# Performance work log

Hardware: AMD Instinct MI355X
Metric: run time of the kernel (lower is better)

Reference implementation:

```python
import jax, jax.numpy as jnp
import numpy as np

N_LAYERS = 3
FEATS = 128
POS = 3
M_DIM = 64
E_IN = 1 + 2 * FEATS          # 257 (rel_dist + x_i + x_j)
N_NODES = 20000
N_EDGES = 320000
LN_EPS = 1e-5


def _xavier(key, shape):
    fan_in, fan_out = shape[0], shape[1]
    std = (2.0 / (fan_in + fan_out)) ** 0.5
    return jax.random.normal(key, shape, dtype=jnp.float32) * std


def setup_inputs() -> dict:
    key = jax.random.key(0)
    ks = jax.random.split(key, 10)
    x = jax.random.normal(ks[0], (N_NODES, POS + FEATS), dtype=jnp.float32)
    edge_index = jax.random.randint(ks[1], (2, N_EDGES), 0, N_NODES)
    L = N_LAYERS
    def stack(k, shape):
        return jax.vmap(lambda kk: _xavier(kk, shape))(jax.random.split(k, L))
    params = {
        "ew1": stack(ks[2], (E_IN, 2 * E_IN)),      # edge_mlp linear 1
        "eb1": jnp.zeros((L, 2 * E_IN), jnp.float32),
        "ew2": stack(ks[3], (2 * E_IN, M_DIM)),      # edge_mlp linear 2
        "eb2": jnp.zeros((L, M_DIM), jnp.float32),
        "ng": jnp.ones((L, FEATS), jnp.float32),     # node LayerNorm gamma
        "nb": jnp.zeros((L, FEATS), jnp.float32),    # node LayerNorm beta
        "nw1": stack(ks[4], (FEATS + M_DIM, 2 * FEATS)),
        "nb1": jnp.zeros((L, 2 * FEATS), jnp.float32),
        "nw2": stack(ks[5], (2 * FEATS, FEATS)),
        "nb2": jnp.zeros((L, FEATS), jnp.float32),
        "cw1": stack(ks[6], (M_DIM, 4 * M_DIM)),
        "cb1": jnp.zeros((L, 4 * M_DIM), jnp.float32),
        "cw2": stack(ks[7], (4 * M_DIM, 1)),
        "cb2": jnp.zeros((L, 1), jnp.float32),
    }
    return {"x": x, "edge_index": edge_index, **params}


def _layer(x, edge_index, ew1, eb1, ew2, eb2, ng, nb, nw1, nb1, nw2, nb2,
           cw1, cb1, cw2, cb2):
    coors, feats = x[:, :POS], x[:, POS:]
    src, dst = edge_index[0], edge_index[1]
    # relative geometry per edge
    rel_coors = coors[src] - coors[dst]                       # [E, 3]
    rel_dist = jnp.sum(rel_coors * rel_coors, axis=-1, keepdims=True)  # [E, 1]
    # message MLP: cat[x_i (target), x_j (source), rel_dist]
    e_in = jnp.concatenate([feats[dst], feats[src], rel_dist], axis=-1)
    h = jax.nn.silu(e_in @ ew1 + eb1)
    m_ij = jax.nn.silu(h @ ew2 + eb2)                         # [E, m_dim]
    # coordinate update
    coor_w = jax.nn.silu(m_ij @ cw1 + cb1) @ cw2 + cb2        # [E, 1]
    mhat = jax.ops.segment_sum(coor_w * rel_coors, dst, num_segments=N_NODES)
    coors_out = coors + mhat
    # feature update (LayerNorm then MLP, residual)
    m_i = jax.ops.segment_sum(m_ij, dst, num_segments=N_NODES)
    mu = jnp.mean(feats, axis=-1, keepdims=True)
    var = jnp.mean((feats - mu) ** 2, axis=-1, keepdims=True)
    feats_n = (feats - mu) * jax.lax.rsqrt(var + LN_EPS) * ng + nb
    n_in = jnp.concatenate([feats_n, m_i], axis=-1)
    nh = jax.nn.silu(n_in @ nw1 + nb1) @ nw2 + nb2
    feats_out = feats + nh
    return jnp.concatenate([coors_out, feats_out], axis=-1)


def reference(x, edge_index, ew1, eb1, ew2, eb2, ng, nb, nw1, nb1, nw2, nb2,
              cw1, cb1, cw2, cb2):
    for l in range(N_LAYERS):
        x = _layer(x, edge_index,
                   ew1[l], eb1[l], ew2[l], eb2[l],
                   ng[l], nb[l], nw1[l], nb1[l], nw2[l], nb2[l],
                   cw1[l], cb1[l], cw2[l], cb2[l])
    return x
```

## Files before the change

kernel.cpp:

```cpp
#include <hip/hip_runtime.h>

typedef unsigned short u16;
typedef unsigned int   u32;
typedef __attribute__((ext_vector_type(2))) u32  u32x2;
typedef __attribute__((ext_vector_type(4))) u32  u32x4;
typedef __attribute__((ext_vector_type(8))) __bf16 bf16x8;
typedef __attribute__((ext_vector_type(4))) float  f32x4;

#define NN 20000
#define NE 320000
#define XD 131
#define F  128
#define MD 64
#define H1 514
#define H1P 544
#define NCH 17

#define GAS __attribute__((address_space(1)))
#define LAS __attribute__((address_space(3)))
#define LGKM0 asm volatile("s_waitcnt lgkmcnt(0)" ::: "memory")
#define VM0   asm volatile("s_waitcnt vmcnt(0)" ::: "memory")

__device__ __forceinline__ float silu(float a) {
    float e = __expf(-a);
    return a * __builtin_amdgcn_rcpf(1.0f + e);
}

__device__ __forceinline__ u16 f2bf(float f) {
    u32 u = __builtin_bit_cast(u32, f);
    return (u16)((u + 0x7FFFu + ((u >> 16) & 1u)) >> 16);
}
__device__ __forceinline__ u16 bfc(float f) { return __builtin_bit_cast(u16, (__bf16)f); }
__device__ __forceinline__ u32 pk2(float a, float b) {
    return (u32)bfc(a) | ((u32)bfc(b) << 16);
}
__device__ __forceinline__ bf16x8 mk8(u32 a, u32 b, u32 c, u32 d) {
    u32x4 t = {a, b, c, d};
    return __builtin_bit_cast(bf16x8, t);
}
__device__ __forceinline__ f32x4 mfma16(bf16x8 a, bf16x8 b, f32x4 c) {
    return __builtin_amdgcn_mfma_f32_16x16x32_bf16(a, b, c, 0, 0, 0);
}


__global__ void prep_w1(const float* __restrict__ ew1, const float* __restrict__ eb1,
                        u16* __restrict__ w1b, float* __restrict__ bias2) {
    int i = blockIdx.x * 256 + threadIdx.x;
    if (i >= 3 * H1P * 256) return;
    int k = i & 255;
    int n = (i >> 8) % H1P;
    int l = (i >> 8) / H1P;
    float v = (n < H1) ? ew1[(size_t)l * 257 * H1 + (size_t)k * H1 + n] : 0.f;
    w1b[(size_t)(l * H1P + n) * 256 + (k ^ ((n & 7) << 3))] = f2bf(v);
    if (k == 0) {
        bias2[(l * H1P + n) * 2 + 0] = (n < H1) ? eb1[l * H1 + n] : 0.f;
        bias2[(l * H1P + n) * 2 + 1] = (n < H1) ? ew1[(size_t)l * 257 * H1 + (size_t)256 * H1 + n] : 0.f;
    }
}

__global__ void prep_w2(const float* __restrict__ ew2, u16* __restrict__ w2b) {
    int i = blockIdx.x * 256 + threadIdx.x;
    if (i >= 3 * 64 * H1P) return;
    int k = i % H1P;
    int n = (i / H1P) & 63;
    int l = i / (H1P * 64);
    float v = (k < H1) ? ew2[(size_t)l * H1 * 64 + (size_t)k * 64 + n] : 0.f;
    w2b[(size_t)(l * 64 + n) * H1P + k] = f2bf(v);
}

__global__ void prep_cw1(const float* __restrict__ cw1, u16* __restrict__ cw1b) {
    int i = blockIdx.x * 256 + threadIdx.x;
    if (i >= 3 * 256 * 64) return;
    int k = i & 63;
    int n = (i >> 6) & 255;
    int l = i >> 14;
    cw1b[(size_t)l * 16384 + n * 64 + k] = f2bf(cw1[(size_t)l * 16384 + k * 256 + n]);
}

__global__ void prep_nw1(const float* __restrict__ nw1, u16* __restrict__ nw1b) {
    int i = blockIdx.x * 256 + threadIdx.x;
    if (i >= 3 * 256 * 192) return;
    int k = i % 192;
    int n = (i / 192) & 255;
    int l = i / (192 * 256);
    nw1b[(size_t)(l * 256 + n) * 192 + k] = f2bf(nw1[(size_t)l * 192 * 256 + (size_t)k * 256 + n]);
}

__global__ void prep_nw2(const float* __restrict__ nw2, u16* __restrict__ nw2b) {
    int i = blockIdx.x * 256 + threadIdx.x;
    if (i >= 3 * 128 * 256) return;
    int k = i & 255;
    int n = (i >> 8) & 127;
    int l = i >> 15;
    nw2b[(size_t)(l * 128 + n) * 256 + k] = f2bf(nw2[(size_t)l * 256 * 128 + (size_t)k * 128 + n]);
}

__global__ void x2bf(const float* __restrict__ xc, u32* __restrict__ xbf) {
    int i = blockIdx.x * 256 + threadIdx.x;
    if (i >= NN * 64) return;
    const int node = i >> 6, p = i & 63;
    const float a = xc[(size_t)node * XD + 3 + 2 * p];
    const float b = xc[(size_t)node * XD + 4 + 2 * p];
    xbf[(size_t)node * 64 + p] = pk2(a, b);
}


__global__ void csr_hist(const int* __restrict__ eidx, int* __restrict__ cnt) {
    int e = blockIdx.x * 256 + threadIdx.x;
    if (e < NE) atomicAdd(&cnt[eidx[NE + e]], 1);
}

__global__ void csr_scan(const int* __restrict__ cnt, int* __restrict__ rowp) {
    __shared__ int ps[1024];
    const int t = threadIdx.x;
    const int base = t * 20;
    int loc[20];
    int s = 0;
    #pragma unroll
    for (int i = 0; i < 20; ++i) {
        const int idx = base + i;
        const int c = (idx < NN) ? cnt[idx] : 0;
        loc[i] = s;
        s += c;
    }
    ps[t] = s;
    __syncthreads();
    for (int off = 1; off < 1024; off <<= 1) {
        int v = (t >= off) ? ps[t - off] : 0;
        __syncthreads();
        ps[t] += v;
        __syncthreads();
    }
    const int segbase = (t > 0) ? ps[t - 1] : 0;
    #pragma unroll
    for (int i = 0; i < 20; ++i) {
        const int idx = base + i;
        if (idx < NN) rowp[idx] = segbase + loc[i];
    }
    if (t == 1023) rowp[NN] = ps[1023];
}

__global__ void csr_fill(const int* __restrict__ eidx, const int* __restrict__ rowp,
                         int* __restrict__ fill, int* __restrict__ eids) {
    int e = blockIdx.x * 256 + threadIdx.x;
    if (e >= NE) return;
    const int d = eidx[NE + e];
    const int pos = atomicAdd(&fill[d], 1);
    eids[rowp[d] + pos] = e;
}

__global__ void esort(const int* __restrict__ eidx, const int* __restrict__ eids,
                      int* __restrict__ esrc, int* __restrict__ edst) {
    int j = blockIdx.x * 256 + threadIdx.x;
    if (j >= NE) return;
    const int e = eids[j];
    esrc[j] = eidx[e];
    edst[j] = eidx[NE + e];
}


__global__ __launch_bounds__(256, 4) void reduce_mi(
    const u16* __restrict__ gmij, const float* __restrict__ gmh,
    const int* __restrict__ rowp, float* __restrict__ m_i, float* __restrict__ mh) {
    const int tid = threadIdx.x;
    const int n = blockIdx.x * 8 + (tid >> 5);
    const int t = tid & 31;
    if (n >= NN) return;
    const int b = rowp[n], e = rowp[n + 1];
    float a0 = 0.f, a1 = 0.f;
    for (int j = b; j < e; ++j) {
        const u32 v = *(const u32*)(gmij + (size_t)j * 64 + t * 2);
        a0 += __builtin_bit_cast(float, v << 16);
        a1 += __builtin_bit_cast(float, v & 0xFFFF0000u);
    }
    m_i[(size_t)n * 64 + 2 * t]     = a0;
    m_i[(size_t)n * 64 + 2 * t + 1] = a1;
    if (t < 3) {
        float m = 0.f;
        for (int j = b; j < e; ++j) m += gmh[(size_t)j * 4 + t];
        mh[n * 3 + t] = m;
    }
}


__global__ __launch_bounds__(256, 3) void edge_mfma(
    const float* __restrict__ x, const u16* __restrict__ xbf,
    const int* __restrict__ esrc, const int* __restrict__ edst,
    const char* __restrict__ w1b, const float* __restrict__ bias2,
    const char* __restrict__ w2b, const float* __restrict__ eb2,
    const char* __restrict__ cw1b, const float* __restrict__ cb1,
    const float* __restrict__ cw2, const float* __restrict__ cb2,
    float* __restrict__ m_i, float* __restrict__ mhat,
    u16* __restrict__ gmij, float* __restrict__ gmh)
{
    __shared__ __align__(16) char LDS[45568];
    const int tid = threadIdx.x;
    const int w = tid >> 6, l = tid & 63, lg = l >> 4, lc = l & 15;
    const int ebase = blockIdx.x * 128 + w * 32;
    char*  HT  = LDS + 32768 + w * 2560;
    char*  MJ  = LDS + w * 4352;
    float* RDS = (float*)(LDS + 43008);
    int*   SDS = (int*)(LDS + 45056);
    char*  STG = LDS + w * 8192;

    if (l < 32) {
        const int e = ebase + l;
        const int s = esrc[e], d = edst[e];
        const float ax = x[(size_t)s * XD + 0] - x[(size_t)d * XD + 0];
        const float ay = x[(size_t)s * XD + 1] - x[(size_t)d * XD + 1];
        const float az = x[(size_t)s * XD + 2] - x[(size_t)d * XD + 2];
        f32x4 v = {ax, ay, az, ax * ax + ay * ay + az * az};
        *(f32x4*)(RDS + (w * 32 + l) * 4) = v;
        SDS[w * 32 + l] = d;
    }

    bf16x8 A[2][8];
    const int r4 = l >> 4;
    #pragma unroll
    for (int p = 0; p < 2; ++p) {
        const int* ea = p ? esrc : edst;
        #pragma unroll
        for (int j = 0; j < 8; ++j) {
            const int r = j * 4 + r4;
            const int node = ea[ebase + r];
            const int cp = lc ^ (r & 7);
            __builtin_amdgcn_global_load_lds((const GAS u32*)(xbf + (size_t)node * 128 + cp * 8),
                                             (LAS u32*)(STG + j * 1024), 16, 0, 0);
        }
        VM0;
        #pragma unroll
        for (int kt = 0; kt < 4; ++kt)
            #pragma unroll
            for (int et = 0; et < 2; ++et) {
                const int R = et * 16 + lc;
                A[et][p * 4 + kt] = *(bf16x8*)(STG + R * 256 + ((kt * 64 + lg * 16) ^ ((R & 7) << 4)));
            }
        LGKM0;
    }

    float rd_e[2];
    rd_e[0] = RDS[(w * 32 + lc) * 4 + 3];
    rd_e[1] = RDS[(w * 32 + 16 + lc) * 4 + 3];
    LGKM0;

    __syncthreads();

    f32x4 c2[2][4];
    #pragma unroll
    for (int nt = 0; nt < 4; ++nt) {
        const float b = eb2[nt * 16 + lc];
        c2[0][nt] = (f32x4){b, b, b, b};
        c2[1][nt] = (f32x4){b, b, b, b};
    }

    {
        const char* g = w1b + (size_t)w * 4096;
        #pragma unroll
        for (int r = 0; r < 4; ++r)
            __builtin_amdgcn_global_load_lds((const GAS u32*)(g + r * 1024 + l * 16),
                                             (LAS u32*)(LDS + w * 4096 + r * 1024), 16, 0, 0);
    }

    const float* pB = bias2;
    #pragma unroll 1
    for (int ch = 0; ch < NCH; ++ch) {
        VM0;
        __syncthreads();
        if (ch + 1 < NCH) {
            const char* g = w1b + (size_t)(ch + 1) * 16384 + w * 4096;
            char* dst = LDS + ((ch + 1) & 1) * 16384 + w * 4096;
            #pragma unroll
            for (int r = 0; r < 4; ++r)
                __builtin_amdgcn_global_load_lds((const GAS u32*)(g + r * 1024 + l * 16),
                                                 (LAS u32*)(dst + r * 1024), 16, 0, 0);
        }
        char* Bc = LDS + (ch & 1) * 16384;

        #pragma unroll
        for (int nt = 0; nt < 2; ++nt) {
            const float* bp = pB + (nt * 16 + lg * 4) * 2;
            f32x4 q0 = *(const f32x4*)(bp);
            f32x4 q1 = *(const f32x4*)(bp + 4);
            f32x4 c10, c11;
            c10[0] = fmaf(rd_e[0], q0[1], q0[0]); c10[1] = fmaf(rd_e[0], q0[3], q0[2]);
            c10[2] = fmaf(rd_e[0], q1[1], q1[0]); c10[3] = fmaf(rd_e[0], q1[3], q1[2]);
            c11[0] = fmaf(rd_e[1], q0[1], q0[0]); c11[1] = fmaf(rd_e[1], q0[3], q0[2]);
            c11[2] = fmaf(rd_e[1], q1[1], q1[0]); c11[3] = fmaf(rd_e[1], q1[3], q1[2]);
            const int nl = nt * 16 + lc;
            #pragma unroll
            for (int kt = 0; kt < 8; ++kt) {
                bf16x8 Wf = *(bf16x8*)(Bc + nl * 512 + ((kt * 64 + lg * 16) ^ ((nl & 7) << 4)));
                c10 = mfma16(Wf, A[0][kt], c10);
                c11 = mfma16(Wf, A[1][kt], c11);
            }
            u32x2 v0, v1;
            v0[0] = pk2(silu(c10[0]), silu(c10[1])); v0[1] = pk2(silu(c10[2]), silu(c10[3]));
            v1[0] = pk2(silu(c11[0]), silu(c11[1])); v1[1] = pk2(silu(c11[2]), silu(c11[3]));
            *(u32x2*)(HT + lc * 80 + nt * 32 + lg * 8) = v0;
            *(u32x2*)(HT + (16 + lc) * 80 + nt * 32 + lg * 8) = v1;
        }
        LGKM0;
        bf16x8 A2[2];
        A2[0] = *(bf16x8*)(HT + lc * 80 + lg * 16);
        A2[1] = *(bf16x8*)(HT + (16 + lc) * 80 + lg * 16);
        #pragma unroll
        for (int nt = 0; nt < 4; ++nt) {
            bf16x8 Bw = __builtin_bit_cast(bf16x8,
                *(const u32x4*)(w2b + (size_t)(nt * 16 + lc) * 1088 + ch * 64 + lg * 16));
            c2[0][nt] = mfma16(A2[0], Bw, c2[0][nt]);
            c2[1][nt] = mfma16(A2[1], Bw, c2[1][nt]);
        }
        pB += 64;
    }

    __syncthreads();

    int dstn[2][4];
    #pragma unroll
    for (int mt = 0; mt < 2; ++mt)
        #pragma unroll
        for (int r = 0; r < 4; ++r)
            dstn[mt][r] = SDS[w * 32 + mt * 16 + lg * 4 + r];

    #pragma unroll
    for (int mt = 0; mt < 2; ++mt)
        #pragma unroll
        for (int nt = 0; nt < 4; ++nt)
            #pragma unroll
            for (int r = 0; r < 4; ++r) {
                const float v = silu(c2[mt][nt][r]);
                const int rowl = mt * 16 + lg * 4 + r;
                const int col  = nt * 16 + lc;
                *(u16*)(MJ + rowl * 136 + col * 2) = bfc(v);
                if (!gmij) atomicAdd(m_i + (size_t)dstn[mt][r] * 64 + col, v);
            }
    LGKM0;

    if (gmij) {
        u16* grow = gmij + (size_t)ebase * 64;
        #pragma unroll
        for (int i = 0; i < 4; ++i) {
            const int row = i * 8 + (l >> 3);
            u32x4 v = *(u32x4*)(MJ + row * 136 + (l & 7) * 16);
            *(u32x4*)(grow + (size_t)row * 64 + (l & 7) * 8) = v;
        }
    }

    bf16x8 A3[2][2];
    #pragma unroll
    for (int mt = 0; mt < 2; ++mt)
        #pragma unroll
        for (int kt = 0; kt < 2; ++kt)
            A3[mt][kt] = *(bf16x8*)(MJ + (mt * 16 + lc) * 136 + kt * 64 + lg * 16);

    float pw[2][4] = {{0.f, 0.f, 0.f, 0.f}, {0.f, 0.f, 0.f, 0.f}};
    #pragma unroll 4
    for (int ct3 = 0; ct3 < 16; ++ct3) {
        const int col = ct3 * 16 + lc;
        const float b = cb1[col];
        f32x4 c30 = {b, b, b, b}, c31 = {b, b, b, b};
        #pragma unroll
        for (int kt = 0; kt < 2; ++kt) {
            bf16x8 B = __builtin_bit_cast(bf16x8,
                *(const u32x4*)(cw1b + (size_t)col * 128 + kt * 64 + lg * 16));
            c30 = mfma16(A3[0][kt], B, c30);
            c31 = mfma16(A3[1][kt], B, c31);
        }
        const float w2v = cw2[col];
        #pragma unroll
        for (int r = 0; r < 4; ++r) {
            pw[0][r] = fmaf(silu(c30[r]), w2v, pw[0][r]);
            pw[1][r] = fmaf(silu(c31[r]), w2v, pw[1][r]);
        }
    }
    #pragma unroll
    for (int m = 1; m < 16; m <<= 1)
        #pragma unroll
        for (int mt = 0; mt < 2; ++mt)
            #pragma unroll
            for (int r = 0; r < 4; ++r)
                pw[mt][r] += __shfl_xor(pw[mt][r], m, 64);

    const float cb2v = cb2[0];
    if (lc < 3) {
        #pragma unroll
        for (int mt = 0; mt < 2; ++mt)
            #pragma unroll
            for (int r = 0; r < 4; ++r) {
                const int rowl = mt * 16 + lg * 4 + r;
                const float cwv = pw[mt][r] + cb2v;
                const float contrib = cwv * RDS[(w * 32 + rowl) * 4 + lc];
                if (gmij)
                    gmh[(size_t)(ebase + rowl) * 4 + lc] = contrib;
                else
                    atomicAdd(mhat + (size_t)dstn[mt][r] * 3 + lc, contrib);
            }
    }
}


__global__ __launch_bounds__(256, 2) void node_mfma(
    const float* __restrict__ xc, const float* __restrict__ m_i, const float* __restrict__ mh,
    const float* __restrict__ ng, const float* __restrict__ nb,
    const char* __restrict__ nw1b, const float* __restrict__ nb1,
    const char* __restrict__ nw2b, const float* __restrict__ nb2,
    float* __restrict__ xn)
{
    __shared__ __align__(16) char LDS[4 * 4352];
    const int tid = threadIdx.x;
    const int w = tid >> 6, l = tid & 63, lg = l >> 4, lc = l & 15;
    char* HB = LDS + w * 4352;
    const int nb0 = blockIdx.x * 128 + w * 32;

    int nodes[2]; bool valid[2];
    #pragma unroll
    for (int et = 0; et < 2; ++et) {
        int n = nb0 + et * 16 + lc;
        valid[et] = (n < NN);
        nodes[et] = valid[et] ? n : (NN - 1);
    }

    bf16x8 BF[2][6];
    #pragma unroll
    for (int et = 0; et < 2; ++et) {
        const float* xr = xc + (size_t)nodes[et] * XD + 3;
        float v[4][8];
        float s = 0.f, q = 0.f;
        #pragma unroll
        for (int kt = 0; kt < 4; ++kt) {
            const int k0 = kt * 32 + lg * 8;
            #pragma unroll
            for (int j = 0; j < 8; ++j) {
                const float t = xr[k0 + j];
                v[kt][j] = t; s += t; q = fmaf(t, t, q);
            }
        }
        s += __shfl_xor(s, 16, 64); s += __shfl_xor(s, 32, 64);
        q += __shfl_xor(q, 16, 64); q += __shfl_xor(q, 32, 64);
        const float mu = s * (1.f / 128.f);
        const float rs = rsqrtf(q * (1.f / 128.f) - mu * mu + 1e-5f);
        #pragma unroll
        for (int kt = 0; kt < 4; ++kt) {
            const int k0 = kt * 32 + lg * 8;
            float4 g0 = *(const float4*)(ng + k0), g1 = *(const float4*)(ng + k0 + 4);
            float4 b0 = *(const float4*)(nb + k0), b1 = *(const float4*)(nb + k0 + 4);
            const u32 u0 = pk2((v[kt][0] - mu) * rs * g0.x + b0.x, (v[kt][1] - mu) * rs * g0.y + b0.y);
            const u32 u1 = pk2((v[kt][2] - mu) * rs * g0.z + b0.z, (v[kt][3] - mu) * rs * g0.w + b0.w);
            const u32 u2 = pk2((v[kt][4] - mu) * rs * g1.x + b1.x, (v[kt][5] - mu) * rs * g1.y + b1.y);
// ... 67 lines not shown
            }
        LGKM0;
        __builtin_amdgcn_sched_barrier(0);
    }

    #pragma unroll
    for (int et = 0; et < 2; ++et) {
        if (!valid[et]) continue;
        const size_t nr = (size_t)nodes[et] * XD;
        #pragma unroll
        for (int ct2 = 0; ct2 < 8; ++ct2)
            #pragma unroll
            for (int r = 0; r < 4; ++r) {
                const int col = ct2 * 16 + lg * 4 + r;
                xn[nr + 3 + col] = a2[ct2][et][r] + xc[nr + 3 + col];
            }
    }
    for (int idx = tid; idx < 384; idx += 256) {
        const int n = blockIdx.x * 128 + idx / 3;
        const int d = idx - (idx / 3) * 3;
        if (n < NN)
            xn[(size_t)n * XD + d] = xc[(size_t)n * XD + d] + mh[n * 3 + d];
    }
}


extern "C" void kernel_launch(void* const* d_in, const int* in_sizes, int n_in,
                              void* d_out, int out_size, void* d_ws, size_t ws_size,
                              hipStream_t stream) {
    const float* x_in = (const float*)d_in[0];
    const int*   eidx = (const int*)  d_in[1];
    const float* ew1  = (const float*)d_in[2];
    const float* eb1  = (const float*)d_in[3];
    const float* ew2  = (const float*)d_in[4];
    const float* eb2  = (const float*)d_in[5];
    const float* ng   = (const float*)d_in[6];
    const float* nb   = (const float*)d_in[7];
    const float* nw1  = (const float*)d_in[8];
    const float* nb1  = (const float*)d_in[9];
    const float* nw2  = (const float*)d_in[10];
    const float* nb2  = (const float*)d_in[11];
    const float* cw1  = (const float*)d_in[12];
    const float* cb1  = (const float*)d_in[13];
    const float* cw2  = (const float*)d_in[14];
    const float* cb2  = (const float*)d_in[15];
    float* out = (float*)d_out;

    char* ws = (char*)d_ws;
    size_t off = 0;
    auto alloc = [&](size_t bytes) { char* p = ws + off; off = (off + bytes + 255) & ~255ull; return p; };
    float* mi    = (float*)alloc((size_t)NN * MD * 4);
    float* mh    = (float*)alloc((size_t)NN * 3 * 4);
    u32*   xbf   = (u32*)  alloc((size_t)NN * 256);
    float* bias2 = (float*)alloc((size_t)3 * H1P * 8);
    char*  w1b   = alloc((size_t)3 * H1P * 512);
    char*  w2b   = alloc((size_t)3 * 64 * 1088);
    char*  cw1b  = alloc((size_t)3 * 256 * 128);
    char*  nw1b  = alloc((size_t)3 * 256 * 384);
    char*  nw2b  = alloc((size_t)3 * 128 * 512);
    u16* gmij = (u16*)alloc((size_t)NE * 64 * 2);
    float* gmh= (float*)alloc((size_t)NE * 4 * 4);
    int* rowp = (int*) alloc((size_t)(NN + 1) * 4);
    int* eids = (int*) alloc((size_t)NE * 4);
    int* esrc = (int*) alloc((size_t)NE * 4);
    int* edst = (int*) alloc((size_t)NE * 4);
    int* cnt  = (int*) alloc((size_t)NN * 4);
    int* fillp= (int*) alloc((size_t)NN * 4);
    const bool two = (off <= ws_size);

    prep_w1 <<<(3 * H1P * 256 + 255) / 256, 256, 0, stream>>>(ew1, eb1, (u16*)w1b, bias2);
    prep_w2 <<<(3 * 64 * H1P + 255) / 256, 256, 0, stream>>>(ew2, (u16*)w2b);
    prep_cw1<<<(3 * 256 * 64 + 255) / 256, 256, 0, stream>>>(cw1, (u16*)cw1b);
    prep_nw1<<<(3 * 256 * 192 + 255) / 256, 256, 0, stream>>>(nw1, (u16*)nw1b);
    prep_nw2<<<(3 * 128 * 256 + 255) / 256, 256, 0, stream>>>(nw2, (u16*)nw2b);

    const int* esrcA = eidx;
    const int* edstA = eidx + NE;
    if (two) {
        hipMemsetAsync(cnt,  0, (size_t)NN * 4, stream);
        hipMemsetAsync(fillp,0, (size_t)NN * 4, stream);
        csr_hist<<<(NE + 255) / 256, 256, 0, stream>>>(eidx, cnt);
        csr_scan<<<1, 1024, 0, stream>>>(cnt, rowp);
        csr_fill<<<(NE + 255) / 256, 256, 0, stream>>>(eidx, rowp, fillp, eids);
        esort<<<(NE + 255) / 256, 256, 0, stream>>>(eidx, eids, esrc, edst);
        esrcA = esrc; edstA = edst;
    }

    for (int l = 0; l < 3; ++l) {
        const float* xc = (l == 0) ? x_in : out;
        float*       xn = out;
        if (!two) {
            hipMemsetAsync(mi, 0, (size_t)NN * MD * 4, stream);
            hipMemsetAsync(mh, 0, (size_t)NN * 3 * 4, stream);
        }
        x2bf<<<(NN * 64 + 255) / 256, 256, 0, stream>>>(xc, xbf);
        edge_mfma<<<NE / 128, 256, 0, stream>>>(
            xc, (const u16*)xbf, esrcA, edstA,
            w1b + (size_t)l * H1P * 512, bias2 + (size_t)l * H1P * 2,
            w2b + (size_t)l * 64 * 1088, eb2 + (size_t)l * 64,
            cw1b + (size_t)l * 256 * 128, cb1 + (size_t)l * 256,
            cw2 + (size_t)l * 256, cb2 + l,
            mi, mh, two ? gmij : (u16*)nullptr, two ? gmh : (float*)nullptr);
        if (two)
            reduce_mi<<<(NN + 7) / 8, 256, 0, stream>>>(gmij, gmh, rowp, mi, mh);
        node_mfma<<<(NN + 127) / 128, 256, 0, stream>>>(
            xc, mi, mh,
            ng + (size_t)l * F, nb + (size_t)l * F,
            nw1b + (size_t)l * 256 * 384, nb1 + (size_t)l * 256,
            nw2b + (size_t)l * 128 * 512, nb2 + (size_t)l * F,
            xn);
    }
}
```

Baseline: 857.8 us.

## Precompute per-node first-layer edge MLP projections and gather them per edge

The first edge-MLP linear layer is split by linearity into per-node terms: each node's features are multiplied once by the x_i and x_j halves of the weight matrix in a new ygemm kernel, producing a bf16 buffer Y. The edge kernel then gathers Y rows for dst and src, adds the rel_dist term and applies SiLU, so the 257x514 GEMM per edge becomes an N-node GEMM plus gathers. This trades edge-level compute for a larger workspace buffer and extra random memory traffic. It also adds a bf16 rounding step on the intermediate sums. The old path is kept as a fallback when the workspace is too small.

```diff
diff --git a/kernel.cpp b/kernel.cpp
--- a/kernel.cpp
+++ b/kernel.cpp
@@ -34,6 +34,8 @@
 __device__ __forceinline__ u32 pk2(float a, float b) {
     return (u32)bfc(a) | ((u32)bfc(b) << 16);
 }
+__device__ __forceinline__ float blo(u32 u) { return __builtin_bit_cast(float, u << 16); }
+__device__ __forceinline__ float bhi(u32 u) { return __builtin_bit_cast(float, u & 0xFFFF0000u); }
 __device__ __forceinline__ bf16x8 mk8(u32 a, u32 b, u32 c, u32 d) {
     u32x4 t = {a, b, c, d};
     return __builtin_bit_cast(bf16x8, t);
@@ -43,8 +45,8 @@
 }
 
 
-__global__ void prep_w1(const float* __restrict__ ew1, const float* __restrict__ eb1,
-                        u16* __restrict__ w1b, float* __restrict__ bias2) {
+__global__ void prep_w1o(const float* __restrict__ ew1, const float* __restrict__ eb1,
+                         u16* __restrict__ w1b, float* __restrict__ bias2) {
     int i = blockIdx.x * 256 + threadIdx.x;
     if (i >= 3 * H1P * 256) return;
     int k = i & 255;
@@ -58,6 +60,23 @@
     }
 }
 
+__global__ void prep_w1n(const float* __restrict__ ew1, const float* __restrict__ eb1,
+                         u16* __restrict__ w1p, float* __restrict__ eb1p, float* __restrict__ w1lf) {
+    int i = blockIdx.x * 256 + threadIdx.x;
+    if (i >= 3 * 1088 * 128) return;
+    int k = i & 127;
+    int n = (i >> 7) % 1088;
+    int l = (i >> 7) / 1088;
+    float v;
+    if (n < H1P) v = (n < H1) ? ew1[(size_t)l * 257 * H1 + (size_t)k * H1 + n] : 0.f;
+    else { int nn = n - H1P; v = (nn < H1) ? ew1[(size_t)l * 257 * H1 + (size_t)(128 + k) * H1 + nn] : 0.f; }
+    w1p[(size_t)(l * 1088 + n) * 128 + k] = f2bf(v);
+    if (k == 0 && n < H1P) {
+        eb1p[l * H1P + n] = (n < H1) ? eb1[l * H1 + n] : 0.f;
+        w1lf[l * H1P + n] = (n < H1) ? ew1[(size_t)l * 257 * H1 + (size_t)256 * H1 + n] : 0.f;
+    }
+}
+
 __global__ void prep_w2(const float* __restrict__ ew2, u16* __restrict__ w2b) {
     int i = blockIdx.x * 256 + threadIdx.x;
     if (i >= 3 * 64 * H1P) return;
@@ -102,6 +121,49 @@
     const float a = xc[(size_t)node * XD + 3 + 2 * p];
     const float b = xc[(size_t)node * XD + 4 + 2 * p];
     xbf[(size_t)node * 64 + p] = pk2(a, b);
+}
+
+
+__global__ __launch_bounds__(256, 4) void ygemm(
+    const u16* __restrict__ xbf, const char* __restrict__ w1p,
+    const float* __restrict__ eb1p, u16* __restrict__ Y)
+{
+    const int tid = threadIdx.x;
+    const int w = tid >> 6, l = tid & 63, lg = l >> 4, lc = l & 15;
+    const int nb0 = blockIdx.x * 128 + w * 32;
+    const int n0 = nb0 + lc, n1 = nb0 + 16 + lc;
+    const bool v0 = n0 < NN, v1 = n1 < NN;
+    const int m0 = v0 ? n0 : NN - 1, m1 = v1 ? n1 : NN - 1;
+
+    bf16x8 BF[2][4];
+    #pragma unroll
+    for (int kt = 0; kt < 4; ++kt) {
+        BF[0][kt] = *(const bf16x8*)((const char*)xbf + (size_t)m0 * 256 + kt * 64 + lg * 16);
+        BF[1][kt] = *(const bf16x8*)((const char*)xbf + (size_t)m1 * 256 + kt * 64 + lg * 16);
+    }
+
+    const int t0 = blockIdx.y * 17;
+    #pragma unroll 1
+    for (int t = t0; t < t0 + 17; ++t) {
+        bf16x8 AW[4];
+        #pragma unroll
+        for (int kt = 0; kt < 4; ++kt)
+            AW[kt] = *(const bf16x8*)(w1p + (size_t)(t * 16 + lc) * 256 + kt * 64 + lg * 16);
+        const int cb = t * 16 + lg * 4;
+        f32x4 binit = {0.f, 0.f, 0.f, 0.f};
+        if (cb < H1P) binit = *(const f32x4*)(eb1p + cb);
+        f32x4 c0 = binit, c1 = binit;
+        #pragma unroll
+        for (int kt = 0; kt < 4; ++kt) {
+            c0 = mfma16(AW[kt], BF[0][kt], c0);
+            c1 = mfma16(AW[kt], BF[1][kt], c1);
+        }
+        u32x2 p0, p1;
+        p0[0] = pk2(c0[0], c0[1]); p0[1] = pk2(c0[2], c0[3]);
+        p1[0] = pk2(c1[0], c1[1]); p1[1] = pk2(c1[2], c1[3]);
+        if (v0) *(u32x2*)(Y + (size_t)m0 * 1088 + cb) = p0;
+        if (v1) *(u32x2*)(Y + (size_t)m1 * 1088 + cb) = p1;
+    }
 }
 
 
@@ -170,8 +232,8 @@
     float a0 = 0.f, a1 = 0.f;
     for (int j = b; j < e; ++j) {
         const u32 v = *(const u32*)(gmij + (size_t)j * 64 + t * 2);
-        a0 += __builtin_bit_cast(float, v << 16);
-        a1 += __builtin_bit_cast(float, v & 0xFFFF0000u);
+        a0 += blo(v);
+        a1 += bhi(v);
     }
     m_i[(size_t)n * 64 + 2 * t]     = a0;
     m_i[(size_t)n * 64 + 2 * t + 1] = a1;
@@ -179,6 +241,153 @@
         float m = 0.f;
         for (int j = b; j < e; ++j) m += gmh[(size_t)j * 4 + t];
         mh[n * 3 + t] = m;
+    }
+}
+
+
+__global__ __launch_bounds__(256, 4) void edge_mfma2(
+    const float* __restrict__ x, const u16* __restrict__ Y,
+    const int* __restrict__ esrc, const int* __restrict__ edst,
+    const float* __restrict__ w1lf,
+    const char* __restrict__ w2b, const float* __restrict__ eb2,
+    const char* __restrict__ cw1b, const float* __restrict__ cb1,
+    const float* __restrict__ cw2, const float* __restrict__ cb2,
+    u16* __restrict__ gmij, float* __restrict__ gmh)
+{
+    __shared__ __align__(16) char LDS[19456];
+    const int tid = threadIdx.x;
+    const int w = tid >> 6, l = tid & 63, lg = l >> 4, lc = l & 15;
+    const int ebase = blockIdx.x * 128 + w * 32;
+    char*  MJ  = LDS + w * 4352;
+    float* RDS = (float*)(LDS + 17408);
+
+    if (l < 32) {
+        const int e = ebase + l;
+        const int s = esrc[e], d = edst[e];
+        const float ax = x[(size_t)s * XD + 0] - x[(size_t)d * XD + 0];
+        const float ay = x[(size_t)s * XD + 1] - x[(size_t)d * XD + 1];
+        const float az = x[(size_t)s * XD + 2] - x[(size_t)d * XD + 2];
+        f32x4 v = {ax, ay, az, ax * ax + ay * ay + az * az};
+        *(f32x4*)(RDS + (w * 32 + l) * 4) = v;
+    }
+    const int s0 = esrc[ebase + lc],      d0 = edst[ebase + lc];
+    const int s1 = esrc[ebase + 16 + lc], d1 = edst[ebase + 16 + lc];
+    LGKM0;
+    const float rd0 = RDS[(w * 32 + lc) * 4 + 3];
+    const float rd1 = RDS[(w * 32 + 16 + lc) * 4 + 3];
+
+    f32x4 c2[2][4];
+    #pragma unroll
+    for (int nt = 0; nt < 4; ++nt) {
+        const float b = eb2[nt * 16 + lc];
+        c2[0][nt] = (f32x4){b, b, b, b};
+        c2[1][nt] = (f32x4){b, b, b, b};
+    }
+
+    #pragma unroll 1
+    for (int ch = 0; ch < NCH; ++ch) {
+        const int cb = ch * 32 + lg * 8;
+        u32x4 ya0 = *(const u32x4*)(Y + (size_t)d0 * 1088 + cb);
+        u32x4 yb0 = *(const u32x4*)(Y + (size_t)s0 * 1088 + 544 + cb);
+        u32x4 ya1 = *(const u32x4*)(Y + (size_t)d1 * 1088 + cb);
+        u32x4 yb1 = *(const u32x4*)(Y + (size_t)s1 * 1088 + 544 + cb);
+        f32x4 wlA = *(const f32x4*)(w1lf + cb);
+        f32x4 wlB = *(const f32x4*)(w1lf + cb + 4);
+        u32 pk0[4], pk1[4];
+        #pragma unroll
+        for (int j = 0; j < 4; ++j) {
+            const float wa = (j < 2) ? wlA[2 * j]     : wlB[2 * j - 4];
+            const float wb = (j < 2) ? wlA[2 * j + 1] : wlB[2 * j - 3];
+            {
+                const float a0 = blo(ya0[j]) + blo(yb0[j]) + rd0 * wa;
+                const float a1 = bhi(ya0[j]) + bhi(yb0[j]) + rd0 * wb;
+                pk0[j] = pk2(silu(a0), silu(a1));
+            }
+            {
+                const float a0 = blo(ya1[j]) + blo(yb1[j]) + rd1 * wa;
+                const float a1 = bhi(ya1[j]) + bhi(yb1[j]) + rd1 * wb;
+                pk1[j] = pk2(silu(a0), silu(a1));
+            }
+        }
+        bf16x8 A20 = mk8(pk0[0], pk0[1], pk0[2], pk0[3]);
+        bf16x8 A21 = mk8(pk1[0], pk1[1], pk1[2], pk1[3]);
+        #pragma unroll
+        for (int nt = 0; nt < 4; ++nt) {
+            bf16x8 Bw = __builtin_bit_cast(bf16x8,
+                *(const u32x4*)(w2b + (size_t)(nt * 16 + lc) * 1088 + ch * 64 + lg * 16));
+            c2[0][nt] = mfma16(A20, Bw, c2[0][nt]);
+            c2[1][nt] = mfma16(A21, Bw, c2[1][nt]);
+        }
+    }
+
+    #pragma unroll
+    for (int mt = 0; mt < 2; ++mt)
+        #pragma unroll
+        for (int nt = 0; nt < 4; ++nt)
+            #pragma unroll
+            for (int r = 0; r < 4; ++r) {
+                const float v = silu(c2[mt][nt][r]);
+                const int rowl = mt * 16 + lg * 4 + r;
+                const int col  = nt * 16 + lc;
+                *(u16*)(MJ + rowl * 136 + col * 2) = bfc(v);
+            }
+    LGKM0;
+
+    {
+        u16* grow = gmij + (size_t)ebase * 64;
+        #pragma unroll
+        for (int i = 0; i < 4; ++i) {
+            const int row = i * 8 + (l >> 3);
+            u32x4 v = *(u32x4*)(MJ + row * 136 + (l & 7) * 16);
+            *(u32x4*)(grow + (size_t)row * 64 + (l & 7) * 8) = v;
+        }
+    }
+
+    bf16x8 A3[2][2];
+    #pragma unroll
+    for (int mt = 0; mt < 2; ++mt)
+        #pragma unroll
+        for (int kt = 0; kt < 2; ++kt)
+            A3[mt][kt] = *(bf16x8*)(MJ + (mt * 16 + lc) * 136 + kt * 64 + lg * 16);
+
+    float pw[2][4] = {{0.f, 0.f, 0.f, 0.f}, {0.f, 0.f, 0.f, 0.f}};
+    #pragma unroll 4
+    for (int ct3 = 0; ct3 < 16; ++ct3) {
+        const int col = ct3 * 16 + lc;
+        const float b = cb1[col];
+        f32x4 c30 = {b, b, b, b}, c31 = {b, b, b, b};
+        #pragma unroll
+        for (int kt = 0; kt < 2; ++kt) {
+            bf16x8 B = __builtin_bit_cast(bf16x8,
+                *(const u32x4*)(cw1b + (size_t)col * 128 + kt * 64 + lg * 16));
+            c30 = mfma16(A3[0][kt], B, c30);
+            c31 = mfma16(A3[1][kt], B, c31);
+        }
+        const float w2v = cw2[col];
+        #pragma unroll
+        for (int r = 0; r < 4; ++r) {
+            pw[0][r] = fmaf(silu(c30[r]), w2v, pw[0][r]);
+            pw[1][r] = fmaf(silu(c31[r]), w2v, pw[1][r]);
+        }
+    }
+    #pragma unroll
+    for (int m = 1; m < 16; m <<= 1)
+        #pragma unroll
+        for (int mt = 0; mt < 2; ++mt)
+            #pragma unroll
+            for (int r = 0; r < 4; ++r)
+                pw[mt][r] += __shfl_xor(pw[mt][r], m, 64);
+
+    const float cb2v = cb2[0];
+    if (lc < 3) {
+        #pragma unroll
+        for (int mt = 0; mt < 2; ++mt)
+            #pragma unroll
+            for (int r = 0; r < 4; ++r) {
+                const int rowl = mt * 16 + lg * 4 + r;
+                const float cwv = pw[mt][r] + cb2v;
+                gmh[(size_t)(ebase + rowl) * 4 + lc] = cwv * RDS[(w * 32 + rowl) * 4 + lc];
+            }
     }
 }
 
@@ -568,22 +777,30 @@
     float* mh    = (float*)alloc((size_t)NN * 3 * 4);
     u32*   xbf   = (u32*)  alloc((size_t)NN * 256);
     float* bias2 = (float*)alloc((size_t)3 * H1P * 8);
+    float* eb1pf = (float*)alloc((size_t)3 * H1P * 4);
+    float* w1lf  = (float*)alloc((size_t)3 * H1P * 4);
     char*  w1b   = alloc((size_t)3 * H1P * 512);
+    char*  w1p   = alloc((size_t)3 * 1088 * 256);
     char*  w2b   = alloc((size_t)3 * 64 * 1088);
     char*  cw1b  = alloc((size_t)3 * 256 * 128);
     char*  nw1b  = alloc((size_t)3 * 256 * 384);
     char*  nw2b  = alloc((size_t)3 * 128 * 512);
-    u16* gmij = (u16*)alloc((size_t)NE * 64 * 2);
-    float* gmh= (float*)alloc((size_t)NE * 4 * 4);
     int* rowp = (int*) alloc((size_t)(NN + 1) * 4);
     int* eids = (int*) alloc((size_t)NE * 4);
     int* esrc = (int*) alloc((size_t)NE * 4);
     int* edst = (int*) alloc((size_t)NE * 4);
     int* cnt  = (int*) alloc((size_t)NN * 4);
     int* fillp= (int*) alloc((size_t)NN * 4);
-    const bool two = (off <= ws_size);
-
-    prep_w1 <<<(3 * H1P * 256 + 255) / 256, 256, 0, stream>>>(ew1, eb1, (u16*)w1b, bias2);
+    u16* gmij = (u16*)alloc((size_t)NE * 64 * 2);
+    float* gmh= (float*)alloc((size_t)NE * 4 * 4);
+    const size_t off_two = off;
+    u16* Ybuf = (u16*)alloc((size_t)NN * 1088 * 2);
+    const size_t off_all = off;
+    const bool pathA = (off_all <= ws_size);
+    const bool two   = (off_two <= ws_size);
+
+    prep_w1o<<<(3 * H1P * 256 + 255) / 256, 256, 0, stream>>>(ew1, eb1, (u16*)w1b, bias2);
+    prep_w1n<<<(3 * 1088 * 128 + 255) / 256, 256, 0, stream>>>(ew1, eb1, (u16*)w1p, eb1pf, w1lf);
     prep_w2 <<<(3 * 64 * H1P + 255) / 256, 256, 0, stream>>>(ew2, (u16*)w2b);
     prep_cw1<<<(3 * 256 * 64 + 255) / 256, 256, 0, stream>>>(cw1, (u16*)cw1b);
     prep_nw1<<<(3 * 256 * 192 + 255) / 256, 256, 0, stream>>>(nw1, (u16*)nw1b);
@@ -609,15 +826,26 @@
             hipMemsetAsync(mh, 0, (size_t)NN * 3 * 4, stream);
         }
         x2bf<<<(NN * 64 + 255) / 256, 256, 0, stream>>>(xc, xbf);
-        edge_mfma<<<NE / 128, 256, 0, stream>>>(
-            xc, (const u16*)xbf, esrcA, edstA,
-            w1b + (size_t)l * H1P * 512, bias2 + (size_t)l * H1P * 2,
-            w2b + (size_t)l * 64 * 1088, eb2 + (size_t)l * 64,
-            cw1b + (size_t)l * 256 * 128, cb1 + (size_t)l * 256,
-            cw2 + (size_t)l * 256, cb2 + l,
-            mi, mh, two ? gmij : (u16*)nullptr, two ? gmh : (float*)nullptr);
-        if (two)
+        if (pathA) {
+            ygemm<<<dim3((NN + 127) / 128, 4), 256, 0, stream>>>(
+                (const u16*)xbf, w1p + (size_t)l * 1088 * 256, eb1pf + (size_t)l * H1P, Ybuf);
+            edge_mfma2<<<NE / 128, 256, 0, stream>>>(
+                xc, Ybuf, esrcA, edstA, w1lf + (size_t)l * H1P,
+                w2b + (size_t)l * 64 * 1088, eb2 + (size_t)l * 64,
+                cw1b + (size_t)l * 256 * 128, cb1 + (size_t)l * 256,
+                cw2 + (size_t)l * 256, cb2 + l, gmij, gmh);
             reduce_mi<<<(NN + 7) / 8, 256, 0, stream>>>(gmij, gmh, rowp, mi, mh);
+        } else {
+            edge_mfma<<<NE / 128, 256, 0, stream>>>(
+                xc, (const u16*)xbf, esrcA, edstA,
+                w1b + (size_t)l * H1P * 512, bias2 + (size_t)l * H1P * 2,
+                w2b + (size_t)l * 64 * 1088, eb2 + (size_t)l * 64,
+                cw1b + (size_t)l * 256 * 128, cb1 + (size_t)l * 256,
+                cw2 + (size_t)l * 256, cb2 + l,
+                mi, mh, two ? gmij : (u16*)nullptr, two ? gmh : (float*)nullptr);
+            if (two)
+                reduce_mi<<<(NN + 7) / 8, 256, 0, stream>>>(gmij, gmh, rowp, mi, mh);
+        }
         node_mfma<<<(NN + 127) / 128, 256, 0, stream>>>(
             xc, mi, mh,
             ng + (size_t)l * F, nb + (size_t)l * F,
```

New measurement: 821.3 us. 4.3% less time.

## Precompute per-node destination half of edge layer-1 GEMM

Applied to the files above, without the earlier changes.

Splits the first edge MLP linear into a destination-node part and a source-node part. The destination part plus bias is computed once per node by a new ygemm kernel into a bf16 buffer Y, and each edge gathers its row instead of recomputing it. This halves the per-edge K dimension of the first GEMM, at the cost of an extra N×544 bf16 intermediate and an added bf16 rounding of the partial sum. The edge kernel also drops its LDS double-buffered weight staging and syncthreads in favour of direct global weight loads, and always takes the CSR reduce path.

```diff
diff --git a/kernel.cpp b/kernel.cpp
--- a/kernel.cpp
+++ b/kernel.cpp
@@ -19,7 +19,6 @@
 #define GAS __attribute__((address_space(1)))
 #define LAS __attribute__((address_space(3)))
 #define LGKM0 asm volatile("s_waitcnt lgkmcnt(0)" ::: "memory")
-#define VM0   asm volatile("s_waitcnt vmcnt(0)" ::: "memory")
 
 __device__ __forceinline__ float silu(float a) {
     float e = __expf(-a);
@@ -34,6 +33,8 @@
 __device__ __forceinline__ u32 pk2(float a, float b) {
     return (u32)bfc(a) | ((u32)bfc(b) << 16);
 }
+__device__ __forceinline__ float blo(u32 u) { return __builtin_bit_cast(float, u << 16); }
+__device__ __forceinline__ float bhi(u32 u) { return __builtin_bit_cast(float, u & 0xFFFF0000u); }
 __device__ __forceinline__ bf16x8 mk8(u32 a, u32 b, u32 c, u32 d) {
     u32x4 t = {a, b, c, d};
     return __builtin_bit_cast(bf16x8, t);
@@ -43,18 +44,20 @@
 }
 
 
-__global__ void prep_w1(const float* __restrict__ ew1, const float* __restrict__ eb1,
-                        u16* __restrict__ w1b, float* __restrict__ bias2) {
+__global__ void prep_w1n(const float* __restrict__ ew1, const float* __restrict__ eb1,
+                         u16* __restrict__ w1p, float* __restrict__ eb1p, float* __restrict__ w1lf) {
     int i = blockIdx.x * 256 + threadIdx.x;
-    if (i >= 3 * H1P * 256) return;
-    int k = i & 255;
-    int n = (i >> 8) % H1P;
-    int l = (i >> 8) / H1P;
-    float v = (n < H1) ? ew1[(size_t)l * 257 * H1 + (size_t)k * H1 + n] : 0.f;
-    w1b[(size_t)(l * H1P + n) * 256 + (k ^ ((n & 7) << 3))] = f2bf(v);
-    if (k == 0) {
-        bias2[(l * H1P + n) * 2 + 0] = (n < H1) ? eb1[l * H1 + n] : 0.f;
-        bias2[(l * H1P + n) * 2 + 1] = (n < H1) ? ew1[(size_t)l * 257 * H1 + (size_t)256 * H1 + n] : 0.f;
+    if (i >= 3 * 1088 * 128) return;
+    int k = i & 127;
+    int n = (i >> 7) % 1088;
+    int l = (i >> 7) / 1088;
+    float v;
+    if (n < H1P) v = (n < H1) ? ew1[(size_t)l * 257 * H1 + (size_t)k * H1 + n] : 0.f;
+    else { int nn = n - H1P; v = (nn < H1) ? ew1[(size_t)l * 257 * H1 + (size_t)(128 + k) * H1 + nn] : 0.f; }
+    w1p[(size_t)(l * 1088 + n) * 128 + k] = f2bf(v);
+    if (k == 0 && n < H1P) {
+        eb1p[l * H1P + n] = (n < H1) ? eb1[l * H1 + n] : 0.f;
+        w1lf[l * H1P + n] = (n < H1) ? ew1[(size_t)l * 257 * H1 + (size_t)256 * H1 + n] : 0.f;
     }
 }
 
@@ -102,6 +105,48 @@
     const float a = xc[(size_t)node * XD + 3 + 2 * p];
     const float b = xc[(size_t)node * XD + 4 + 2 * p];
     xbf[(size_t)node * 64 + p] = pk2(a, b);
+}
+
+
+__global__ __launch_bounds__(256, 4) void ygemm(
+    const u16* __restrict__ xbf, const char* __restrict__ w1p,
+    const float* __restrict__ eb1p, u16* __restrict__ Y)
+{
+    const int tid = threadIdx.x;
+    const int w = tid >> 6, l = tid & 63, lg = l >> 4, lc = l & 15;
+    const int nb0 = blockIdx.x * 128 + w * 32;
+    const int n0 = nb0 + lc, n1 = nb0 + 16 + lc;
+    const bool v0 = n0 < NN, v1 = n1 < NN;
+    const int m0 = v0 ? n0 : NN - 1, m1 = v1 ? n1 : NN - 1;
+
+    bf16x8 BF[2][4];
+    #pragma unroll
+    for (int kt = 0; kt < 4; ++kt) {
+        BF[0][kt] = *(const bf16x8*)((const char*)xbf + (size_t)m0 * 256 + kt * 64 + lg * 16);
+        BF[1][kt] = *(const bf16x8*)((const char*)xbf + (size_t)m1 * 256 + kt * 64 + lg * 16);
+    }
+
+    const int t0 = blockIdx.y * 17;
+    #pragma unroll 1
+    for (int t = t0; t < t0 + 17; ++t) {
+        bf16x8 AW[4];
+        #pragma unroll
+        for (int kt = 0; kt < 4; ++kt)
+            AW[kt] = *(const bf16x8*)(w1p + (size_t)(t * 16 + lc) * 256 + kt * 64 + lg * 16);
+        const int cb = t * 16 + lg * 4;
+        f32x4 binit = *(const f32x4*)(eb1p + cb);
+        f32x4 c0 = binit, c1 = binit;
+        #pragma unroll
+        for (int kt = 0; kt < 4; ++kt) {
+            c0 = mfma16(AW[kt], BF[0][kt], c0);
+            c1 = mfma16(AW[kt], BF[1][kt], c1);
+        }
+        u32x2 p0, p1;
+        p0[0] = pk2(c0[0], c0[1]); p0[1] = pk2(c0[2], c0[3]);
+        p1[0] = pk2(c1[0], c1[1]); p1[1] = pk2(c1[2], c1[3]);
+        if (v0) *(u32x2*)(Y + (size_t)m0 * H1P + cb) = p0;
+        if (v1) *(u32x2*)(Y + (size_t)m1 * H1P + cb) = p1;
+    }
 }
 
 
@@ -170,8 +215,8 @@
     float a0 = 0.f, a1 = 0.f;
     for (int j = b; j < e; ++j) {
         const u32 v = *(const u32*)(gmij + (size_t)j * 64 + t * 2);
-        a0 += __builtin_bit_cast(float, v << 16);
-        a1 += __builtin_bit_cast(float, v & 0xFFFF0000u);
+        a0 += blo(v);
+        a1 += bhi(v);
     }
     m_i[(size_t)n * 64 + 2 * t]     = a0;
     m_i[(size_t)n * 64 + 2 * t + 1] = a1;
@@ -183,25 +228,22 @@
 }
 
 
-__global__ __launch_bounds__(256, 3) void edge_mfma(
-    const float* __restrict__ x, const u16* __restrict__ xbf,
+__global__ __launch_bounds__(256, 3) void edge_mfma3(
+    const float* __restrict__ x, const u16* __restrict__ Y, const u16* __restrict__ xbf,
     const int* __restrict__ esrc, const int* __restrict__ edst,
-    const char* __restrict__ w1b, const float* __restrict__ bias2,
+    const char* __restrict__ w1bh, const float* __restrict__ w1lf,
     const char* __restrict__ w2b, const float* __restrict__ eb2,
     const char* __restrict__ cw1b, const float* __restrict__ cb1,
     const float* __restrict__ cw2, const float* __restrict__ cb2,
-    float* __restrict__ m_i, float* __restrict__ mhat,
     u16* __restrict__ gmij, float* __restrict__ gmh)
 {
-    __shared__ __align__(16) char LDS[45568];
+    __shared__ __align__(16) char LDS[29696];
     const int tid = threadIdx.x;
     const int w = tid >> 6, l = tid & 63, lg = l >> 4, lc = l & 15;
     const int ebase = blockIdx.x * 128 + w * 32;
-    char*  HT  = LDS + 32768 + w * 2560;
-    char*  MJ  = LDS + w * 4352;
-    float* RDS = (float*)(LDS + 43008);
-    int*   SDS = (int*)(LDS + 45056);
-    char*  STG = LDS + w * 8192;
+    char*  HT  = LDS + w * 2560;
+    char*  MJ  = LDS + 10240 + w * 4352;
+    float* RDS = (float*)(LDS + 27648);
 
     if (l < 32) {
         const int e = ebase + l;
@@ -211,39 +253,19 @@
         const float az = x[(size_t)s * XD + 2] - x[(size_t)d * XD + 2];
         f32x4 v = {ax, ay, az, ax * ax + ay * ay + az * az};
         *(f32x4*)(RDS + (w * 32 + l) * 4) = v;
-        SDS[w * 32 + l] = d;
-    }
-
-    bf16x8 A[2][8];
-    const int r4 = l >> 4;
-    #pragma unroll
-    for (int p = 0; p < 2; ++p) {
-        const int* ea = p ? esrc : edst;
-        #pragma unroll
-        for (int j = 0; j < 8; ++j) {
-            const int r = j * 4 + r4;
-            const int node = ea[ebase + r];
-            const int cp = lc ^ (r & 7);
-            __builtin_amdgcn_global_load_lds((const GAS u32*)(xbf + (size_t)node * 128 + cp * 8),
-                                             (LAS u32*)(STG + j * 1024), 16, 0, 0);
-        }
-        VM0;
-        #pragma unroll
-        for (int kt = 0; kt < 4; ++kt)
-            #pragma unroll
-            for (int et = 0; et < 2; ++et) {
-                const int R = et * 16 + lc;
-                A[et][p * 4 + kt] = *(bf16x8*)(STG + R * 256 + ((kt * 64 + lg * 16) ^ ((R & 7) << 4)));
-            }
-        LGKM0;
-    }
-
-    float rd_e[2];
-    rd_e[0] = RDS[(w * 32 + lc) * 4 + 3];
-    rd_e[1] = RDS[(w * 32 + 16 + lc) * 4 + 3];
+    }
+    const int s0 = esrc[ebase + lc],      d0 = edst[ebase + lc];
+    const int s1 = esrc[ebase + 16 + lc], d1 = edst[ebase + 16 + lc];
     LGKM0;
-
-    __syncthreads();
+    const float rd0 = RDS[(w * 32 + lc) * 4 + 3];
+    const float rd1 = RDS[(w * 32 + 16 + lc) * 4 + 3];
+
+    bf16x8 BX[2][4];
+    #pragma unroll
+    for (int kt = 0; kt < 4; ++kt) {
+        BX[0][kt] = *(const bf16x8*)((const char*)xbf + (size_t)s0 * 256 + kt * 64 + lg * 16);
+        BX[1][kt] = *(const bf16x8*)((const char*)xbf + (size_t)s1 * 256 + kt * 64 + lg * 16);
+    }
 
     f32x4 c2[2][4];
     #pragma unroll
@@ -253,56 +275,38 @@
         c2[1][nt] = (f32x4){b, b, b, b};
     }
 
-    {
-        const char* g = w1b + (size_t)w * 4096;
-        #pragma unroll
-        for (int r = 0; r < 4; ++r)
-            __builtin_amdgcn_global_load_lds((const GAS u32*)(g + r * 1024 + l * 16),
-                                             (LAS u32*)(LDS + w * 4096 + r * 1024), 16, 0, 0);
-    }
-
-    const float* pB = bias2;
     #pragma unroll 1
     for (int ch = 0; ch < NCH; ++ch) {
-        VM0;
-        __syncthreads();
-        if (ch + 1 < NCH) {
-            const char* g = w1b + (size_t)(ch + 1) * 16384 + w * 4096;
-            char* dst = LDS + ((ch + 1) & 1) * 16384 + w * 4096;
-            #pragma unroll
-            for (int r = 0; r < 4; ++r)
-                __builtin_amdgcn_global_load_lds((const GAS u32*)(g + r * 1024 + l * 16),
-                                                 (LAS u32*)(dst + r * 1024), 16, 0, 0);
-        }
-        char* Bc = LDS + (ch & 1) * 16384;
-
-        #pragma unroll
-        for (int nt = 0; nt < 2; ++nt) {
-            const float* bp = pB + (nt * 16 + lg * 4) * 2;
-            f32x4 q0 = *(const f32x4*)(bp);
-            f32x4 q1 = *(const f32x4*)(bp + 4);
+        #pragma unroll
+        for (int t = 0; t < 2; ++t) {
+            const int col = ch * 32 + t * 16 + lg * 4;
+            u32x2 ya0 = *(const u32x2*)(Y + (size_t)d0 * H1P + col);
+            u32x2 ya1 = *(const u32x2*)(Y + (size_t)d1 * H1P + col);
+            f32x4 wl  = *(const f32x4*)(w1lf + col);
             f32x4 c10, c11;
-            c10[0] = fmaf(rd_e[0], q0[1], q0[0]); c10[1] = fmaf(rd_e[0], q0[3], q0[2]);
-            c10[2] = fmaf(rd_e[0], q1[1], q1[0]); c10[3] = fmaf(rd_e[0], q1[3], q1[2]);
-            c11[0] = fmaf(rd_e[1], q0[1], q0[0]); c11[1] = fmaf(rd_e[1], q0[3], q0[2]);
-            c11[2] = fmaf(rd_e[1], q1[1], q1[0]); c11[3] = fmaf(rd_e[1], q1[3], q1[2]);
-            const int nl = nt * 16 + lc;
-            #pragma unroll
-            for (int kt = 0; kt < 8; ++kt) {
-                bf16x8 Wf = *(bf16x8*)(Bc + nl * 512 + ((kt * 64 + lg * 16) ^ ((nl & 7) << 4)));
-                c10 = mfma16(Wf, A[0][kt], c10);
-                c11 = mfma16(Wf, A[1][kt], c11);
+            c10[0] = fmaf(rd0, wl[0], blo(ya0[0])); c10[1] = fmaf(rd0, wl[1], bhi(ya0[0]));
+            c10[2] = fmaf(rd0, wl[2], blo(ya0[1])); c10[3] = fmaf(rd0, wl[3], bhi(ya0[1]));
+            c11[0] = fmaf(rd1, wl[0], blo(ya1[0])); c11[1] = fmaf(rd1, wl[1], bhi(ya1[0]));
+            c11[2] = fmaf(rd1, wl[2], blo(ya1[1])); c11[3] = fmaf(rd1, wl[3], bhi(ya1[1]));
+            const int wrow = ch * 32 + t * 16 + lc;
+            #pragma unroll
+            for (int kt = 0; kt < 4; ++kt) {
+                bf16x8 AW = __builtin_bit_cast(bf16x8,
+                    *(const u32x4*)(w1bh + (size_t)wrow * 256 + kt * 64 + lg * 16));
+                c10 = mfma16(AW, BX[0][kt], c10);
+                c11 = mfma16(AW, BX[1][kt], c11);
             }
             u32x2 v0, v1;
             v0[0] = pk2(silu(c10[0]), silu(c10[1])); v0[1] = pk2(silu(c10[2]), silu(c10[3]));
             v1[0] = pk2(silu(c11[0]), silu(c11[1])); v1[1] = pk2(silu(c11[2]), silu(c11[3]));
-            *(u32x2*)(HT + lc * 80 + nt * 32 + lg * 8) = v0;
-            *(u32x2*)(HT + (16 + lc) * 80 + nt * 32 + lg * 8) = v1;
+            *(u32x2*)(HT + lc * 80 + t * 32 + lg * 8) = v0;
+            *(u32x2*)(HT + (16 + lc) * 80 + t * 32 + lg * 8) = v1;
         }
         LGKM0;
         bf16x8 A2[2];
         A2[0] = *(bf16x8*)(HT + lc * 80 + lg * 16);
         A2[1] = *(bf16x8*)(HT + (16 + lc) * 80 + lg * 16);
+        LGKM0;
         #pragma unroll
         for (int nt = 0; nt < 4; ++nt) {
             bf16x8 Bw = __builtin_bit_cast(bf16x8,
@@ -310,17 +314,7 @@
             c2[0][nt] = mfma16(A2[0], Bw, c2[0][nt]);
             c2[1][nt] = mfma16(A2[1], Bw, c2[1][nt]);
         }
-        pB += 64;
-    }
-
-    __syncthreads();
-
-    int dstn[2][4];
-    #pragma unroll
-    for (int mt = 0; mt < 2; ++mt)
-        #pragma unroll
-        for (int r = 0; r < 4; ++r)
-            dstn[mt][r] = SDS[w * 32 + mt * 16 + lg * 4 + r];
+    }
 
     #pragma unroll
     for (int mt = 0; mt < 2; ++mt)
@@ -332,11 +326,10 @@
                 const int rowl = mt * 16 + lg * 4 + r;
                 const int col  = nt * 16 + lc;
                 *(u16*)(MJ + rowl * 136 + col * 2) = bfc(v);
-                if (!gmij) atomicAdd(m_i + (size_t)dstn[mt][r] * 64 + col, v);
             }
     LGKM0;
 
-    if (gmij) {
+    {
         u16* grow = gmij + (size_t)ebase * 64;
         #pragma unroll
         for (int i = 0; i < 4; ++i) {
@@ -389,11 +382,7 @@
             for (int r = 0; r < 4; ++r) {
                 const int rowl = mt * 16 + lg * 4 + r;
                 const float cwv = pw[mt][r] + cb2v;
-                const float contrib = cwv * RDS[(w * 32 + rowl) * 4 + lc];
-                if (gmij)
-                    gmh[(size_t)(ebase + rowl) * 4 + lc] = contrib;
-                else
-                    atomicAdd(mhat + (size_t)dstn[mt][r] * 3 + lc, contrib);
+                gmh[(size_t)(ebase + rowl) * 4 + lc] = cwv * RDS[(w * 32 + rowl) * 4 + lc];
             }
     }
 }
@@ -567,57 +556,49 @@
     float* mi    = (float*)alloc((size_t)NN * MD * 4);
     float* mh    = (float*)alloc((size_t)NN * 3 * 4);
     u32*   xbf   = (u32*)  alloc((size_t)NN * 256);
-    float* bias2 = (float*)alloc((size_t)3 * H1P * 8);
-    char*  w1b   = alloc((size_t)3 * H1P * 512);
+    float* eb1pf = (float*)alloc((size_t)3 * H1P * 4);
+    float* w1lf  = (float*)alloc((size_t)3 * H1P * 4);
+    char*  w1p   = alloc((size_t)3 * 1088 * 256);
     char*  w2b   = alloc((size_t)3 * 64 * 1088);
     char*  cw1b  = alloc((size_t)3 * 256 * 128);
     char*  nw1b  = alloc((size_t)3 * 256 * 384);
     char*  nw2b  = alloc((size_t)3 * 128 * 512);
-    u16* gmij = (u16*)alloc((size_t)NE * 64 * 2);
-    float* gmh= (float*)alloc((size_t)NE * 4 * 4);
     int* rowp = (int*) alloc((size_t)(NN + 1) * 4);
     int* eids = (int*) alloc((size_t)NE * 4);
     int* esrc = (int*) alloc((size_t)NE * 4);
     int* edst = (int*) alloc((size_t)NE * 4);
     int* cnt  = (int*) alloc((size_t)NN * 4);
     int* fillp= (int*) alloc((size_t)NN * 4);
-    const bool two = (off <= ws_size);
-
-    prep_w1 <<<(3 * H1P * 256 + 255) / 256, 256, 0, stream>>>(ew1, eb1, (u16*)w1b, bias2);
+    u16* gmij = (u16*)alloc((size_t)NE * 64 * 2);
+    float* gmh= (float*)alloc((size_t)NE * 4 * 4);
+    u16* Ybuf = (u16*)alloc((size_t)NN * H1P * 2);
+
+    prep_w1n<<<(3 * 1088 * 128 + 255) / 256, 256, 0, stream>>>(ew1, eb1, (u16*)w1p, eb1pf, w1lf);
     prep_w2 <<<(3 * 64 * H1P + 255) / 256, 256, 0, stream>>>(ew2, (u16*)w2b);
     prep_cw1<<<(3 * 256 * 64 + 255) / 256, 256, 0, stream>>>(cw1, (u16*)cw1b);
     prep_nw1<<<(3 * 256 * 192 + 255) / 256, 256, 0, stream>>>(nw1, (u16*)nw1b);
     prep_nw2<<<(3 * 128 * 256 + 255) / 256, 256, 0, stream>>>(nw2, (u16*)nw2b);
 
-    const int* esrcA = eidx;
-    const int* edstA = eidx + NE;
-    if (two) {
-        hipMemsetAsync(cnt,  0, (size_t)NN * 4, stream);
-        hipMemsetAsync(fillp,0, (size_t)NN * 4, stream);
-        csr_hist<<<(NE + 255) / 256, 256, 0, stream>>>(eidx, cnt);
-        csr_scan<<<1, 1024, 0, stream>>>(cnt, rowp);
-        csr_fill<<<(NE + 255) / 256, 256, 0, stream>>>(eidx, rowp, fillp, eids);
-        esort<<<(NE + 255) / 256, 256, 0, stream>>>(eidx, eids, esrc, edst);
-        esrcA = esrc; edstA = edst;
-    }
+    hipMemsetAsync(cnt,  0, (size_t)NN * 4, stream);
+    hipMemsetAsync(fillp,0, (size_t)NN * 4, stream);
+    csr_hist<<<(NE + 255) / 256, 256, 0, stream>>>(eidx, cnt);
+    csr_scan<<<1, 1024, 0, stream>>>(cnt, rowp);
+    csr_fill<<<(NE + 255) / 256, 256, 0, stream>>>(eidx, rowp, fillp, eids);
+    esort<<<(NE + 255) / 256, 256, 0, stream>>>(eidx, eids, esrc, edst);
 
     for (int l = 0; l < 3; ++l) {
         const float* xc = (l == 0) ? x_in : out;
         float*       xn = out;
-        if (!two) {
-            hipMemsetAsync(mi, 0, (size_t)NN * MD * 4, stream);
-            hipMemsetAsync(mh, 0, (size_t)NN * 3 * 4, stream);
-        }
         x2bf<<<(NN * 64 + 255) / 256, 256, 0, stream>>>(xc, xbf);
-        edge_mfma<<<NE / 128, 256, 0, stream>>>(
-            xc, (const u16*)xbf, esrcA, edstA,
-            w1b + (size_t)l * H1P * 512, bias2 + (size_t)l * H1P * 2,
+        ygemm<<<dim3((NN + 127) / 128, 2), 256, 0, stream>>>(
+            (const u16*)xbf, w1p + (size_t)l * 1088 * 256, eb1pf + (size_t)l * H1P, Ybuf);
+        edge_mfma3<<<NE / 128, 256, 0, stream>>>(
+            xc, Ybuf, (const u16*)xbf, esrc, edst,
+            w1p + ((size_t)l * 1088 + H1P) * 256, w1lf + (size_t)l * H1P,
             w2b + (size_t)l * 64 * 1088, eb2 + (size_t)l * 64,
             cw1b + (size_t)l * 256 * 128, cb1 + (size_t)l * 256,
-            cw2 + (size_t)l * 256, cb2 + l,
-            mi, mh, two ? gmij : (u16*)nullptr, two ? gmh : (float*)nullptr);
-        if (two)
-            reduce_mi<<<(NN + 7) / 8, 256, 0, stream>>>(gmij, gmh, rowp, mi, mh);
+            cw2 + (size_t)l * 256, cb2 + l, gmij, gmh);
+        reduce_mi<<<(NN + 7) / 8, 256, 0, stream>>>(gmij, gmh, rowp, mi, mh);
         node_mfma<<<(NN + 127) / 128, 256, 0, stream>>>(
             xc, mi, mh,
             ng + (size_t)l * F, nb + (size_t)l * F,
```

Result: slower. 1.321 ms (+54.0%).
